# Kernel tuning notes

Hardware: AMD Instinct MI355X
Metric: run time of the kernel (lower is better)

## Reference

```python
import jax, jax.numpy as jnp
import numpy as np

REGULARIZE = 1e-4  # minimum eigenvalue clamp, matches precision_pool default
N_CHILD, N_PARENT, K_DIM = 4096, 128, 16


def setup_inputs() -> dict:
    key = jax.random.key(0)
    k1, k2, k3, k4 = jax.random.split(key, 4)
    N, M, K = N_CHILD, N_PARENT, K_DIM
    mu_children = jax.random.normal(k1, (N, K), dtype=jnp.float32)
    # SPD child covariances: A A^T + I
    A = 0.3 * jax.random.normal(k2, (N, K, K), dtype=jnp.float32)
    sigma_children = A @ jnp.swapaxes(A, -1, -2) + jnp.eye(K, dtype=jnp.float32)
    weights = jax.random.uniform(k3, (N, M), dtype=jnp.float32)
    # near-identity invertible transports Omega_{alpha i}: (M, N, K, K)
    transport = 0.1 * jax.random.normal(k4, (M, N, K, K), dtype=jnp.float32) \
        + jnp.eye(K, dtype=jnp.float32)
    return {"mu_children": mu_children, "sigma_children": sigma_children,
            "weights": weights, "transport": transport}


def reference(mu_children, sigma_children, weights, transport):
    """precision_pool vmapped over M meta-agents.

    mu_children: (N, K); sigma_children: (N, K, K);
    weights: (N, M); transport: (M, N, K, K)
    Returns (mu_pooled (M, K), sigma_pooled (M, K, K)).
    """
    # Child precisions Lambda_i = Sigma_i^{-1}
    Lambda_c = jnp.linalg.inv(sigma_children)                      # (N, K, K)
    # Transported precisions Omega Lambda Omega^T: (M, N, K, K)
    Lt = jnp.einsum('mnij,njk,mnlk->mnil', transport, Lambda_c, transport)
    # Precision-weighted sum over children: Lambda_alpha = sum_i w_i Lt_i
    Lp = jnp.einsum('nm,mnij->mij', weights, Lt)                   # (M, K, K)
    Lp = 0.5 * (Lp + jnp.swapaxes(Lp, -1, -2))                     # symmetrize
    # Eigen-clamp for numerical stability, then reconstruct
    evals, evecs = jnp.linalg.eigh(Lp)
    evals = jnp.maximum(evals, REGULARIZE)
    Lp = jnp.einsum('mij,mj,mkj->mik', evecs, evals, evecs)        # (M, K, K)
    # Transported means and information vector
    mu_t = jnp.einsum('mnij,nj->mni', transport, mu_children)      # (M, N, K)
    info = jnp.einsum('nm,mnij,mnj->mi', weights, Lt, mu_t)        # (M, K)
    sigma_pooled = jnp.linalg.inv(Lp)                              # (M, K, K)
    mu_pooled = jnp.einsum('mij,mj->mi', sigma_pooled, info)       # (M, K)
    return mu_pooled, sigma_pooled
```

## Files before the change

kernel.cpp:

```cpp
#include <hip/hip_runtime.h>
#include <hip/hip_bf16.h>

#define NCH   4096
#define NPAR  128
#define KD    16
#define CHUNK 128
#define NCHUNK (NCH / CHUNK)
#define PITCH 24

typedef __attribute__((ext_vector_type(4))) float f4;
typedef __attribute__((ext_vector_type(8))) short bh8;
typedef __attribute__((ext_vector_type(4))) int   i4;
typedef __attribute__((ext_vector_type(2))) unsigned int u2;

static __device__ __forceinline__ unsigned pk2(float a, float b) {
  float2 t; t.x = a; t.y = b;
  union { __hip_bfloat162 h2; unsigned u; } cv;
  cv.h2 = __float22bfloat162_rn(t);
  return cv.u;
}
static __device__ __forceinline__ float bflo(unsigned v) { return __uint_as_float(v << 16); }
static __device__ __forceinline__ float bfhi(unsigned v) { return __uint_as_float(v & 0xFFFF0000u); }

__global__ __launch_bounds__(256) void invert_sigma(const float* __restrict__ sig,
                                                    unsigned short* __restrict__ lam) {
  __shared__ float A[16][17];
  __shared__ float B[16][17];
  const int n = blockIdx.x;
  const int t = threadIdx.x, i = t >> 4, j = t & 15;
  A[i][j] = sig[(size_t)n * 256 + t];
  B[i][j] = (i == j) ? 1.0f : 0.0f;
  __syncthreads();
  for (int k = 0; k < 16; ++k) {
    const float ip  = 1.0f / A[k][k];
    const float akj = A[k][j] * ip;
    const float bkj = B[k][j] * ip;
    const float f   = A[i][k];
    __syncthreads();
    if (i == k) { A[i][j] = akj;      B[i][j] = bkj; }
    else        { A[i][j] -= f * akj; B[i][j] -= f * bkj; }
    __syncthreads();
  }
  __hip_bfloat16 h = __float2bfloat16(B[i][j]);
  lam[(size_t)n * 256 + t] = *reinterpret_cast<unsigned short*>(&h);
}

__global__ __launch_bounds__(256) void pool_pairs(
    const float* __restrict__ transport,
    const unsigned short* __restrict__ lam,
    const float* __restrict__ mu,
    const float* __restrict__ weights,
    float* __restrict__ Lp,
    float* __restrict__ info) {
  __shared__ unsigned short sOm[4][16 * PITCH];
  __shared__ unsigned short sLm[4][16 * PITCH];
  __shared__ float sMu[CHUNK * 16];
  __shared__ float sW[CHUNK];
  __shared__ float sRedLp[4][256];
  __shared__ float sRedIn[4][16];

  const int bx = blockIdx.x;
  const int m  = bx & (NPAR - 1);
  const int c  = bx >> 7;
  const int tid = threadIdx.x;
  const int w = tid >> 6;
  const int L = tid & 63;
  const int q = L >> 4;
  const int t = L & 15;

  #pragma unroll
  for (int r = 0; r < (CHUNK * 16) / 256; ++r) {
    const int idx = r * 256 + tid;
    sMu[idx] = mu[(size_t)c * CHUNK * 16 + idx];
  }
  if (tid < CHUNK) sW[tid] = weights[(size_t)(c * CHUNK + tid) * NPAR + m];
  __syncthreads();

  const int PER_WAVE = CHUNK / 4;
  const int n0 = c * CHUNK + w * PER_WAVE;
  unsigned short* om = sOm[w];
  unsigned short* lm = sLm[w];

  const int wr_off = (L >> 2) * PITCH + (L & 3) * 4;
  const int rd_off = t * PITCH + q * 8;

  f4 accLp = {0.f, 0.f, 0.f, 0.f};
  f4 accIn = {0.f, 0.f, 0.f, 0.f};
  const f4 zf = {0.f, 0.f, 0.f, 0.f};

  const float* tbase = transport + ((size_t)m * NCH + n0) * 256;
  const unsigned short* lbase = lam + (size_t)n0 * 256;

  f4 omNext = *(const f4*)(tbase + 4 * L);
  u2 lmNext = *(const u2*)(lbase + 4 * L);

  for (int it = 0; it < PER_WAVE; ++it) {
    const f4 omv = omNext;
    const u2 lmv = lmNext;
    const int itn = (it + 1 < PER_WAVE) ? it + 1 : it;
    omNext = *(const f4*)(tbase + (size_t)itn * 256 + 4 * L);
    lmNext = *(const u2*)(lbase + (size_t)itn * 256 + 4 * L);
    const int nloc = w * PER_WAVE + it;

    u2 omp; omp.x = pk2(omv.x, omv.y); omp.y = pk2(omv.z, omv.w);
    *(u2*)(om + wr_off) = omp;
    *(u2*)(lm + wr_off) = lmv;
    __builtin_amdgcn_wave_barrier();

    i4 aOmI = {0, 0, 0, 0}, aLmI = {0, 0, 0, 0};
    if (q < 2) {
      aOmI = *(const i4*)(om + rd_off);
      aLmI = *(const i4*)(lm + rd_off);
    }
    union { i4 i; bh8 h; } cvo, cvl, cvp;
    cvo.i = aOmI; cvl.i = aLmI;

    const float* muv = sMu + nloc * 16 + (q & 1) * 8;
    const f4 mlo = *(const f4*)(muv);
    const f4 mhi = *(const f4*)(muv + 4);
    const unsigned a0 = (unsigned)aOmI.x, a1 = (unsigned)aOmI.y,
                   a2 = (unsigned)aOmI.z, a3 = (unsigned)aOmI.w;
    float p = bflo(a0) * mlo.x + bfhi(a0) * mlo.y + bflo(a1) * mlo.z + bfhi(a1) * mlo.w +
              bflo(a2) * mhi.x + bfhi(a2) * mhi.y + bflo(a3) * mhi.z + bfhi(a3) * mhi.w;
    p += __shfl_xor(p, 16, 64);
    p += __shfl_xor(p, 32, 64);

    f4 P = __builtin_amdgcn_mfma_f32_16x16x32_bf16(cvl.h, cvo.h, zf, 0, 0, 0);

    const unsigned pkLoV = pk2(P.x, P.y);
    const unsigned pkHiV = pk2(P.z, P.w);
    const int srcA = t + (q & 1) * 32;
    int w0 = __shfl((int)pkLoV, srcA, 64);
    int w1 = __shfl((int)pkHiV, srcA, 64);
    int w2 = __shfl((int)pkLoV, srcA + 16, 64);
    int w3 = __shfl((int)pkHiV, srcA + 16, 64);
    i4 bPI;
    bPI.x = (q < 2) ? w0 : 0;
    bPI.y = (q < 2) ? w1 : 0;
    bPI.z = (q < 2) ? w2 : 0;
    bPI.w = (q < 2) ? w3 : 0;
    cvp.i = bPI;

    f4 Ct = __builtin_amdgcn_mfma_f32_16x16x32_bf16(cvo.h, cvp.h, zf, 0, 0, 0);

    const float wv = sW[nloc];
    const float wmu = wv * p;
    accLp.x += wv * Ct.x;  accIn.x += wmu * Ct.x;
    accLp.y += wv * Ct.y;  accIn.y += wmu * Ct.y;
    accLp.z += wv * Ct.z;  accIn.z += wmu * Ct.z;
    accLp.w += wv * Ct.w;  accIn.w += wmu * Ct.w;
    __builtin_amdgcn_wave_barrier();
  }

  sRedLp[w][(q * 4 + 0) * 16 + t] = accLp.x;
  sRedLp[w][(q * 4 + 1) * 16 + t] = accLp.y;
  sRedLp[w][(q * 4 + 2) * 16 + t] = accLp.z;
  sRedLp[w][(q * 4 + 3) * 16 + t] = accLp.w;

  float i0 = accIn.x, i1 = accIn.y, i2 = accIn.z, i3 = accIn.w;
  #pragma unroll
  for (int off = 1; off < 16; off <<= 1) {
    i0 += __shfl_xor(i0, off, 64);
    i1 += __shfl_xor(i1, off, 64);
    i2 += __shfl_xor(i2, off, 64);
    i3 += __shfl_xor(i3, off, 64);
  }
  if (t == 0) {
    sRedIn[w][q * 4 + 0] = i0;
    sRedIn[w][q * 4 + 1] = i1;
    sRedIn[w][q * 4 + 2] = i2;
    sRedIn[w][q * 4 + 3] = i3;
  }
  __syncthreads();

  const float s = sRedLp[0][tid] + sRedLp[1][tid] + sRedLp[2][tid] + sRedLp[3][tid];
  atomicAdd(&Lp[(size_t)m * 256 + tid], s);
  if (tid < 16) {
    const float si = sRedIn[0][tid] + sRedIn[1][tid] + sRedIn[2][tid] + sRedIn[3][tid];
    atomicAdd(&info[(size_t)m * 16 + tid], si);
  }
}

__global__ __launch_bounds__(256) void finalize(const float* __restrict__ Lp,
                                                const float* __restrict__ info,
                                                float* __restrict__ out) {
  __shared__ float A[16][17];
  __shared__ float B[16][17];
  __shared__ float infoS[16];
  const int m = blockIdx.x;
  const int tid = threadIdx.x, i = tid >> 4, j = tid & 15;
  const float* Lm = Lp + (size_t)m * 256;
  A[i][j] = 0.5f * (Lm[i * 16 + j] + Lm[j * 16 + i]);
  B[i][j] = (i == j) ? 1.0f : 0.0f;
  if (tid < 16) infoS[tid] = info[(size_t)m * 16 + tid];
  __syncthreads();
  for (int k = 0; k < 16; ++k) {
    const float ip  = 1.0f / A[k][k];
    const float akj = A[k][j] * ip;
    const float bkj = B[k][j] * ip;
    const float f   = A[i][k];
    __syncthreads();
    if (i == k) { A[i][j] = akj;      B[i][j] = bkj; }
    else        { A[i][j] -= f * akj; B[i][j] -= f * bkj; }
    __syncthreads();
  }
  out[(size_t)KD * NPAR + (size_t)m * 256 + tid] = B[i][j];
  if (tid < 16) {
    float s = 0.f;
    #pragma unroll
    for (int jj = 0; jj < 16; ++jj) s += B[tid][jj] * infoS[jj];
    out[(size_t)m * 16 + tid] = s;
  }
}

extern "C" void kernel_launch(void* const* d_in, const int* in_sizes, int n_in,
                              void* d_out, int out_size, void* d_ws, size_t ws_size,
                              hipStream_t stream) {
  const float* mu_children    = (const float*)d_in[0];
  const float* sigma_children = (const float*)d_in[1];
  const float* weights        = (const float*)d_in[2];
  const float* transport      = (const float*)d_in[3];
  float* out = (float*)d_out;

  unsigned short* lam = (unsigned short*)d_ws;
  float* Lp   = (float*)((char*)d_ws + (size_t)NCH * 256 * sizeof(unsigned short));
  float* info = Lp + (size_t)NPAR * 256;

  hipMemsetAsync(Lp, 0, (size_t)(NPAR * 256 + NPAR * 16) * sizeof(float), stream);
  invert_sigma<<<NCH, 256, 0, stream>>>(sigma_children, lam);
  pool_pairs<<<NPAR * NCHUNK, 256, 0, stream>>>(transport, lam, mu_children, weights, Lp, info);
  finalize<<<NPAR, 256, 0, stream>>>(Lp, info, out);
}
```

Before: 697.1 us.

## Load MFMA operands directly from global, drop LDS staging, double-buffer prefetch

```diff
diff --git a/kernel.cpp b/kernel.cpp
--- a/kernel.cpp
+++ b/kernel.cpp
@@ -6,12 +6,10 @@
 #define KD    16
 #define CHUNK 128
 #define NCHUNK (NCH / CHUNK)
-#define PITCH 24
 
 typedef __attribute__((ext_vector_type(4))) float f4;
 typedef __attribute__((ext_vector_type(8))) short bh8;
 typedef __attribute__((ext_vector_type(4))) int   i4;
-typedef __attribute__((ext_vector_type(2))) unsigned int u2;
 
 static __device__ __forceinline__ unsigned pk2(float a, float b) {
   float2 t; t.x = a; t.y = b;
@@ -19,8 +17,6 @@
   cv.h2 = __float22bfloat162_rn(t);
   return cv.u;
 }
-static __device__ __forceinline__ float bflo(unsigned v) { return __uint_as_float(v << 16); }
-static __device__ __forceinline__ float bfhi(unsigned v) { return __uint_as_float(v & 0xFFFF0000u); }
 
 __global__ __launch_bounds__(256) void invert_sigma(const float* __restrict__ sig,
                                                     unsigned short* __restrict__ lam) {
@@ -52,8 +48,6 @@
     const float* __restrict__ weights,
     float* __restrict__ Lp,
     float* __restrict__ info) {
-  __shared__ unsigned short sOm[4][16 * PITCH];
-  __shared__ unsigned short sLm[4][16 * PITCH];
   __shared__ float sMu[CHUNK * 16];
   __shared__ float sW[CHUNK];
   __shared__ float sRedLp[4][256];
@@ -78,78 +72,116 @@
 
   const int PER_WAVE = CHUNK / 4;
   const int n0 = c * CHUNK + w * PER_WAVE;
-  unsigned short* om = sOm[w];
-  unsigned short* lm = sLm[w];
-
-  const int wr_off = (L >> 2) * PITCH + (L & 3) * 4;
-  const int rd_off = t * PITCH + q * 8;
+
+  const int  foff = t * 16 + q * 8;
+  const bool act  = (q < 2);
+
+  const float*          tb = transport + ((size_t)m * NCH + n0) * 256 + foff;
+  const unsigned short* lb = lam + (size_t)n0 * 256 + foff;
+  const float*          muq = sMu + (q & 1) * 8;
 
   f4 accLp = {0.f, 0.f, 0.f, 0.f};
   f4 accIn = {0.f, 0.f, 0.f, 0.f};
   const f4 zf = {0.f, 0.f, 0.f, 0.f};
 
-  const float* tbase = transport + ((size_t)m * NCH + n0) * 256;
-  const unsigned short* lbase = lam + (size_t)n0 * 256;
-
-  f4 omNext = *(const f4*)(tbase + 4 * L);
-  u2 lmNext = *(const u2*)(lbase + 4 * L);
-
-  for (int it = 0; it < PER_WAVE; ++it) {
-    const f4 omv = omNext;
-    const u2 lmv = lmNext;
-    const int itn = (it + 1 < PER_WAVE) ? it + 1 : it;
-    omNext = *(const f4*)(tbase + (size_t)itn * 256 + 4 * L);
-    lmNext = *(const u2*)(lbase + (size_t)itn * 256 + 4 * L);
-    const int nloc = w * PER_WAVE + it;
-
-    u2 omp; omp.x = pk2(omv.x, omv.y); omp.y = pk2(omv.z, omv.w);
-    *(u2*)(om + wr_off) = omp;
-    *(u2*)(lm + wr_off) = lmv;
-    __builtin_amdgcn_wave_barrier();
-
-    i4 aOmI = {0, 0, 0, 0}, aLmI = {0, 0, 0, 0};
-    if (q < 2) {
-      aOmI = *(const i4*)(om + rd_off);
-      aLmI = *(const i4*)(lm + rd_off);
+  f4 oA0 = zf, oA1 = zf, oB0 = zf, oB1 = zf;
+  i4 lA = {0, 0, 0, 0}, lB = {0, 0, 0, 0};
+  if (act) {
+    oA0 = *(const f4*)(tb + 0);
+    oA1 = *(const f4*)(tb + 4);
+    lA  = *(const i4*)(lb + 0);
+    oB0 = *(const f4*)(tb + 256);
+    oB1 = *(const f4*)(tb + 260);
+    lB  = *(const i4*)(lb + 256);
+  }
+
+  const int srcA = t + (q & 1) * 32;
+
+  for (int it = 0; it < PER_WAVE; it += 2) {
+    {
+      const int nloc = w * PER_WAVE + it;
+      union { i4 i; bh8 h; } co, cl, cp;
+      co.i.x = (int)pk2(oA0.x, oA0.y);
+      co.i.y = (int)pk2(oA0.z, oA0.w);
+      co.i.z = (int)pk2(oA1.x, oA1.y);
+      co.i.w = (int)pk2(oA1.z, oA1.w);
+      cl.i = lA;
+
+      const float* mv = muq + nloc * 16;
+      const f4 m0 = *(const f4*)(mv);
+      const f4 m1 = *(const f4*)(mv + 4);
+      float p = oA0.x * m0.x + oA0.y * m0.y + oA0.z * m0.z + oA0.w * m0.w +
+                oA1.x * m1.x + oA1.y * m1.y + oA1.z * m1.z + oA1.w * m1.w;
+
+      const int ia = (it + 2 < PER_WAVE) ? it + 2 : it;
+      if (act) {
+        oA0 = *(const f4*)(tb + (size_t)ia * 256);
+        oA1 = *(const f4*)(tb + (size_t)ia * 256 + 4);
+        lA  = *(const i4*)(lb + (size_t)ia * 256);
+      }
+
+      p += __shfl_xor(p, 16, 64);
+      p += __shfl_xor(p, 32, 64);
+
+      f4 P = __builtin_amdgcn_mfma_f32_16x16x32_bf16(cl.h, co.h, zf, 0, 0, 0);
+      const unsigned pLo = pk2(P.x, P.y);
+      const unsigned pHi = pk2(P.z, P.w);
+      cp.i.x = __shfl((int)pLo, srcA, 64);
+      cp.i.y = __shfl((int)pHi, srcA, 64);
+      cp.i.z = __shfl((int)pLo, srcA + 16, 64);
+      cp.i.w = __shfl((int)pHi, srcA + 16, 64);
+
+      f4 Ct = __builtin_amdgcn_mfma_f32_16x16x32_bf16(co.h, cp.h, zf, 0, 0, 0);
+
+      const float wv  = sW[nloc];
+      const float wmu = wv * p;
+      accLp.x += wv * Ct.x;  accIn.x += wmu * Ct.x;
+      accLp.y += wv * Ct.y;  accIn.y += wmu * Ct.y;
+      accLp.z += wv * Ct.z;  accIn.z += wmu * Ct.z;
+      accLp.w += wv * Ct.w;  accIn.w += wmu * Ct.w;
     }
-    union { i4 i; bh8 h; } cvo, cvl, cvp;
-    cvo.i = aOmI; cvl.i = aLmI;
-
-    const float* muv = sMu + nloc * 16 + (q & 1) * 8;
-    const f4 mlo = *(const f4*)(muv);
-    const f4 mhi = *(const f4*)(muv + 4);
-    const unsigned a0 = (unsigned)aOmI.x, a1 = (unsigned)aOmI.y,
-                   a2 = (unsigned)aOmI.z, a3 = (unsigned)aOmI.w;
-    float p = bflo(a0) * mlo.x + bfhi(a0) * mlo.y + bflo(a1) * mlo.z + bfhi(a1) * mlo.w +
-              bflo(a2) * mhi.x + bfhi(a2) * mhi.y + bflo(a3) * mhi.z + bfhi(a3) * mhi.w;
-    p += __shfl_xor(p, 16, 64);
-    p += __shfl_xor(p, 32, 64);
-
-    f4 P = __builtin_amdgcn_mfma_f32_16x16x32_bf16(cvl.h, cvo.h, zf, 0, 0, 0);
-
-    const unsigned pkLoV = pk2(P.x, P.y);
-    const unsigned pkHiV = pk2(P.z, P.w);
-    const int srcA = t + (q & 1) * 32;
-    int w0 = __shfl((int)pkLoV, srcA, 64);
-    int w1 = __shfl((int)pkHiV, srcA, 64);
-    int w2 = __shfl((int)pkLoV, srcA + 16, 64);
-    int w3 = __shfl((int)pkHiV, srcA + 16, 64);
-    i4 bPI;
-    bPI.x = (q < 2) ? w0 : 0;
-    bPI.y = (q < 2) ? w1 : 0;
-    bPI.z = (q < 2) ? w2 : 0;
-    bPI.w = (q < 2) ? w3 : 0;
-    cvp.i = bPI;
-
-    f4 Ct = __builtin_amdgcn_mfma_f32_16x16x32_bf16(cvo.h, cvp.h, zf, 0, 0, 0);
-
-    const float wv = sW[nloc];
-    const float wmu = wv * p;
-    accLp.x += wv * Ct.x;  accIn.x += wmu * Ct.x;
-    accLp.y += wv * Ct.y;  accIn.y += wmu * Ct.y;
-    accLp.z += wv * Ct.z;  accIn.z += wmu * Ct.z;
-    accLp.w += wv * Ct.w;  accIn.w += wmu * Ct.w;
-    __builtin_amdgcn_wave_barrier();
+    {
+      const int nloc = w * PER_WAVE + it + 1;
+      union { i4 i; bh8 h; } co, cl, cp;
+      co.i.x = (int)pk2(oB0.x, oB0.y);
+      co.i.y = (int)pk2(oB0.z, oB0.w);
+      co.i.z = (int)pk2(oB1.x, oB1.y);
+      co.i.w = (int)pk2(oB1.z, oB1.w);
+      cl.i = lB;
+
+      const float* mv = muq + nloc * 16;
+      const f4 m0 = *(const f4*)(mv);
+      const f4 m1 = *(const f4*)(mv + 4);
+      float p = oB0.x * m0.x + oB0.y * m0.y + oB0.z * m0.z + oB0.w * m0.w +
+                oB1.x * m1.x + oB1.y * m1.y + oB1.z * m1.z + oB1.w * m1.w;
+
+      const int ib = (it + 3 < PER_WAVE) ? it + 3 : it + 1;
+      if (act) {
+        oB0 = *(const f4*)(tb + (size_t)ib * 256);
+        oB1 = *(const f4*)(tb + (size_t)ib * 256 + 4);
+        lB  = *(const i4*)(lb + (size_t)ib * 256);
+      }
+
+      p += __shfl_xor(p, 16, 64);
+      p += __shfl_xor(p, 32, 64);
+
+      f4 P = __builtin_amdgcn_mfma_f32_16x16x32_bf16(cl.h, co.h, zf, 0, 0, 0);
+      const unsigned pLo = pk2(P.x, P.y);
+      const unsigned pHi = pk2(P.z, P.w);
+      cp.i.x = __shfl((int)pLo, srcA, 64);
+      cp.i.y = __shfl((int)pHi, srcA, 64);
+      cp.i.z = __shfl((int)pLo, srcA + 16, 64);
+      cp.i.w = __shfl((int)pHi, srcA + 16, 64);
+
+      f4 Ct = __builtin_amdgcn_mfma_f32_16x16x32_bf16(co.h, cp.h, zf, 0, 0, 0);
+
+      const float wv  = sW[nloc];
+      const float wmu = wv * p;
+      accLp.x += wv * Ct.x;  accIn.x += wmu * Ct.x;
+      accLp.y += wv * Ct.y;  accIn.y += wmu * Ct.y;
+      accLp.z += wv * Ct.z;  accIn.z += wmu * Ct.z;
+      accLp.w += wv * Ct.w;  accIn.w += wmu * Ct.w;
+    }
   }
 
   sRedLp[w][(q * 4 + 0) * 16 + t] = accLp.x;
```

New measurement: 708.6 us. Within noise of the previous version (+1.7%).
